# Performance work log

Hardware: AMD Instinct MI355X
Metric: run time of the kernel (lower is better)

The kernel has to match this reference:

```python
import jax, jax.numpy as jnp
import numpy as np

B = 4096
D_IN = 2048
D_H = 2048
W_SCALE = 0.02  # keep exp() gate pre-activations small / numerically safe


def setup_inputs() -> dict:
    key = jax.random.key(0)
    ks = jax.random.split(key, 16)
    inp = {
        "x": jax.random.normal(ks[0], (B, D_IN), jnp.float32),
        "h_prev": jax.random.normal(ks[1], (B, D_H), jnp.float32),
        "c_prev": jax.random.normal(ks[2], (B, D_H), jnp.float32),
        "n_prev": jax.random.uniform(ks[3], (B, D_H), jnp.float32),
    }
    # input->hidden weights (stored [in, out]; torch Linear computes x @ W.T + b,
    # equivalent to x @ W_here + b) and biases
    for i, name in enumerate(["i", "f", "o", "z"]):
        inp[f"W_{name}"] = jax.random.normal(ks[4 + i], (D_IN, D_H), jnp.float32) * W_SCALE
        inp[f"b_{name}"] = jax.random.normal(ks[8 + i], (D_H,), jnp.float32) * W_SCALE
        inp[f"U_{name}"] = jax.random.normal(ks[12 + i], (D_H, D_H), jnp.float32) * W_SCALE
    return inp


def reference(x, h_prev, c_prev, n_prev,
              W_i, b_i, U_i, W_f, b_f, U_f,
              W_o, b_o, U_o, W_z, b_z, U_z):
    # Gate pre-activations: 8 GEMMs fused pairwise per gate
    i = jnp.exp(x @ W_i + b_i + h_prev @ U_i)
    f = jnp.exp(x @ W_f + b_f + h_prev @ U_f)
    o = jax.nn.sigmoid(x @ W_o + b_o + h_prev @ U_o)
    z = jnp.tanh(x @ W_z + b_z + h_prev @ U_z)
    c = f * c_prev + i * z
    n = f * n_prev + i
    h = o * (c / (n + 1e-6))
    return (h, c, n)
```

## Files before the change

### kernel.cpp

```cpp
#include <hip/hip_runtime.h>
#include <hip/hip_bf16.h>
#include <stdint.h>

#define B_DIM 4096
#define DH    2048
#define K_DIM 4096
#define N_DIM 8192
#define NT    128

typedef __bf16  bf16x8 __attribute__((ext_vector_type(8)));
typedef float   f32x4  __attribute__((ext_vector_type(4)));

__device__ __forceinline__ unsigned short f2bf(float f) {
  unsigned int u = __float_as_uint(f);
  u += 0x7FFFu + ((u >> 16) & 1u);
  return (unsigned short)(u >> 16);
}

__global__ void cast_cat_A(const float* __restrict__ x, const float* __restrict__ h,
                           unsigned short* __restrict__ Abuf) {
  int idx = blockIdx.x * 256 + threadIdx.x;
  const int half = B_DIM * (DH / 4);
  bool isx = (idx < half);
  int i2 = isx ? idx : idx - half;
  int b  = i2 >> 9;
  int c4 = i2 & 511;
  const float* src = (isx ? x : h) + (((size_t)b) << 11) + (c4 << 2);
  float4 v = *(const float4*)src;
  ushort4 o;
  o.x = f2bf(v.x); o.y = f2bf(v.y); o.z = f2bf(v.z); o.w = f2bf(v.w);
  int col = (isx ? 0 : DH) + (c4 << 2);
  *(ushort4*)(Abuf + (size_t)b * K_DIM + col) = o;
}

__global__ void transpose_cast_B(const float* __restrict__ Wi, const float* __restrict__ Ui,
                                 const float* __restrict__ Wf, const float* __restrict__ Uf,
                                 const float* __restrict__ Wo, const float* __restrict__ Uo,
                                 const float* __restrict__ Wz, const float* __restrict__ Uz,
                                 unsigned short* __restrict__ Bt) {
  __shared__ unsigned short lds[64 * 68];
  const int k0 = blockIdx.x * 64;
  const int g  = blockIdx.y >> 5;
  const int j0 = (blockIdx.y & 31) * 64;
  const float* W = (g == 0) ? Wi : (g == 1) ? Wf : (g == 2) ? Wo : Wz;
  const float* U = (g == 0) ? Ui : (g == 1) ? Uf : (g == 2) ? Uo : Uz;
  const float* src = ((k0 < DH) ? (W + (size_t)k0 * DH)
                                : (U + (size_t)(k0 - DH) * DH)) + j0;
  const int t = threadIdx.x;
  #pragma unroll
  for (int r = 0; r < 4; ++r) {
    int slot = r * 256 + t;
    int kk = slot >> 4;
    int c4 = slot & 15;
    float4 v = *(const float4*)(src + (size_t)kk * DH + (c4 << 2));
    int n = c4 << 2;
    lds[(n + 0) * 68 + kk] = f2bf(v.x);
    lds[(n + 1) * 68 + kk] = f2bf(v.y);
    lds[(n + 2) * 68 + kk] = f2bf(v.z);
    lds[(n + 3) * 68 + kk] = f2bf(v.w);
  }
  __syncthreads();
  #pragma unroll
  for (int r = 0; r < 4; ++r) {
    int slot = r * 256 + t;
    int nn = slot >> 4;
    int c8 = slot & 15;
    int j  = j0 + nn;
    int np = ((j >> 5) << 7) + ((j & 16) << 2) + (g << 4) + (j & 15);
    *(ushort4*)(Bt + (size_t)np * K_DIM + k0 + (c8 << 2)) =
        *(const ushort4*)(lds + nn * 68 + (c8 << 2));
  }
}

__global__ __launch_bounds__(512, 2) void gemm_gates(const unsigned short* __restrict__ A,
                                                     const unsigned short* __restrict__ Bt,
                                                     const float* __restrict__ bi, const float* __restrict__ bf,
                                                     const float* __restrict__ bo, const float* __restrict__ bz,
                                                     const float* __restrict__ cprev, const float* __restrict__ nprev,
                                                     float* __restrict__ out) {
  __shared__ alignas(16) unsigned short lds[65536];
  unsigned short* As = lds;
  unsigned short* Bs = lds + 32768;

  const int t    = threadIdx.x;
  const int w    = t >> 6;
  const int lane = t & 63;
  const int lm   = lane & 15;
  const int kg   = lane >> 4;
  const int wm   = w >> 2;
  const int wn   = w & 3;

  const int flat = blockIdx.y * 32 + blockIdx.x;
  const int swzb = (flat & 7) * 64 + (flat >> 3);
  const int bx   = swzb & 31;
  const int by   = swzb >> 5;
  const int m0   = by * 256;
  const int n0   = bx * 256;

  const int r4 = lane >> 2, c4 = lane & 3;
  const int rowS0 = w * 32 + r4;
  const int rowS1 = rowS0 + 16;
  const int kby0 = (c4 * 16) ^ (((rowS0 >> 1) & 3) << 4);
  const int kby1 = (c4 * 16) ^ (((rowS1 >> 1) & 3) << 4);
  const unsigned short* pa0 = A  + (size_t)(m0 + rowS0) * K_DIM + (kby0 >> 1);
  const unsigned short* pa1 = A  + (size_t)(m0 + rowS1) * K_DIM + (kby1 >> 1);
  const unsigned short* pb0 = Bt + (size_t)(n0 + rowS0) * K_DIM + (kby0 >> 1);
  const unsigned short* pb1 = Bt + (size_t)(n0 + rowS1) * K_DIM + (kby1 >> 1);
  const int ldsQ0 = (w * 32) * 32;
  const int ldsQ1 = (w * 32 + 16) * 32;

  const int aoff = (wm * 128 + lm) * 64 + ((kg * 16) ^ (((lm >> 1) & 3) << 4));
  const int boff = (wn * 64  + lm) * 64 + ((kg * 16) ^ (((lm >> 1) & 3) << 4));
  const char* Asc = (const char*)As;
  const char* Bsc = (const char*)Bs;

  f32x4 acc[8][4] = {};

#define STAGE(tile) do {                                                                              \
    const int _buf = (tile) & 3;                                                                      \
    const size_t _k = (size_t)(tile) * 32;                                                            \
    __builtin_amdgcn_global_load_lds((const __attribute__((address_space(1))) unsigned int*)(pa0 + _k), \
        (__attribute__((address_space(3))) unsigned int*)(As + _buf * 8192 + ldsQ0), 16, 0, 0);       \
    __builtin_amdgcn_global_load_lds((const __attribute__((address_space(1))) unsigned int*)(pa1 + _k), \
        (__attribute__((address_space(3))) unsigned int*)(As + _buf * 8192 + ldsQ1), 16, 0, 0);       \
    __builtin_amdgcn_global_load_lds((const __attribute__((address_space(1))) unsigned int*)(pb0 + _k), \
        (__attribute__((address_space(3))) unsigned int*)(Bs + _buf * 8192 + ldsQ0), 16, 0, 0);       \
    __builtin_amdgcn_global_load_lds((const __attribute__((address_space(1))) unsigned int*)(pb1 + _k), \
        (__attribute__((address_space(3))) unsigned int*)(Bs + _buf * 8192 + ldsQ1), 16, 0, 0);       \
  } while (0)

  STAGE(0); STAGE(1); STAGE(2);
  asm volatile("s_waitcnt vmcnt(8)" ::: "memory");
  __builtin_amdgcn_s_barrier();
  asm volatile("" ::: "memory");

  for (int kt = 0; kt < NT; ++kt) {
    const int cur = kt & 3;
    if (kt + 3 < NT) STAGE(kt + 3);

    const char* ab = Asc + cur * 16384 + aoff;
    const char* bb = Bsc + cur * 16384 + boff;

    bf16x8 av[4], bv[4];
    #pragma unroll
    for (int ni = 0; ni < 4; ++ni) bv[ni] = *(const bf16x8*)(bb + ni * 1024);

    #pragma unroll
    for (int i = 0; i < 4; ++i) av[i] = *(const bf16x8*)(ab + i * 1024);
    __builtin_amdgcn_s_setprio(1);
    #pragma unroll
    for (int i = 0; i < 4; ++i)
      #pragma unroll
      for (int ni = 0; ni < 4; ++ni)
        acc[i][ni] = __builtin_amdgcn_mfma_f32_16x16x32_bf16(av[i], bv[ni], acc[i][ni], 0, 0, 0);
    __builtin_amdgcn_s_setprio(0);

    #pragma unroll
    for (int i = 0; i < 4; ++i) av[i] = *(const bf16x8*)(ab + 4096 + i * 1024);
    __builtin_amdgcn_s_setprio(1);
    #pragma unroll
    for (int i = 0; i < 4; ++i)
      #pragma unroll
      for (int ni = 0; ni < 4; ++ni)
        acc[4 + i][ni] = __builtin_amdgcn_mfma_f32_16x16x32_bf16(av[i], bv[ni], acc[4 + i][ni], 0, 0, 0);
    __builtin_amdgcn_s_setprio(0);

    if (kt + 3 < NT)      asm volatile("s_waitcnt vmcnt(8)" ::: "memory");
    else if (kt + 2 < NT) asm volatile("s_waitcnt vmcnt(4)" ::: "memory");
    else                  asm volatile("s_waitcnt vmcnt(0)" ::: "memory");
    __builtin_amdgcn_s_barrier();
    asm volatile("" ::: "memory");
  }

  const int jj = bx * 64 + (wn >> 1) * 32 + (wn & 1) * 16 + lm;
  const float vbi = bi[jj], vbf = bf[jj], vbo = bo[jj], vbz = bz[jj];
  #pragma unroll
  for (int mi = 0; mi < 8; ++mi) {
    const int mrow = m0 + wm * 128 + mi * 16 + kg * 4;
    #pragma unroll
    for (int r = 0; r < 4; ++r) {
      const size_t idx = (size_t)(mrow + r) * DH + jj;
      float pi = acc[mi][0][r] + vbi;
      float pf = acc[mi][1][r] + vbf;
      float po = acc[mi][2][r] + vbo;
      float pz = acc[mi][3][r] + vbz;
      float iv = __expf(pi);
      float fv = __expf(pf);
      float ov = 1.0f / (1.0f + __expf(-po));
      float t2 = __expf(2.0f * pz);
      float zv = 1.0f - 2.0f / (t2 + 1.0f);
      float cv = fv * cprev[idx] + iv * zv;
      float nv = fv * nprev[idx] + iv;
      out[idx]            = ov * (cv / (nv + 1e-6f));
      out[8388608 + idx]  = cv;
      out[16777216 + idx] = nv;
    }
  }
#undef STAGE
}

extern "C" void kernel_launch(void* const* d_in, const int* in_sizes, int n_in,
                              void* d_out, int out_size, void* d_ws, size_t ws_size,
                              hipStream_t stream) {
  const float* x      = (const float*)d_in[0];
  const float* h_prev = (const float*)d_in[1];
  const float* c_prev = (const float*)d_in[2];
  const float* n_prev = (const float*)d_in[3];
  const float* W_i = (const float*)d_in[4];  const float* b_i = (const float*)d_in[5];  const float* U_i = (const float*)d_in[6];
  const float* W_f = (const float*)d_in[7];  const float* b_f = (const float*)d_in[8];  const float* U_f = (const float*)d_in[9];
  const float* W_o = (const float*)d_in[10]; const float* b_o = (const float*)d_in[11]; const float* U_o = (const float*)d_in[12];
  const float* W_z = (const float*)d_in[13]; const float* b_z = (const float*)d_in[14]; const float* U_z = (const float*)d_in[15];
  float* out = (float*)d_out;

  char* ws = (char*)d_ws;
  unsigned short* Abuf = (unsigned short*)ws;
  unsigned short* Bt   = (unsigned short*)(ws + 33554432);

  cast_cat_A<<<16384, 256, 0, stream>>>(x, h_prev, Abuf);
  transpose_cast_B<<<dim3(64, 128), 256, 0, stream>>>(W_i, U_i, W_f, U_f, W_o, U_o, W_z, U_z, Bt);
  gemm_gates<<<dim3(32, 16), 512, 0, stream>>>(Abuf, Bt, b_i, b_f, b_o, b_z, c_prev, n_prev, out);
}
```

Measured before the change: 557.5 us.

## Split global-to-LDS staging around MFMA phases and vectorize transpose LDS writes

Measured after the change: 571.6 us. +2.5%, slower.

```diff
diff --git a/kernel.cpp b/kernel.cpp
--- a/kernel.cpp
+++ b/kernel.cpp
@@ -46,18 +46,22 @@
   const float* U = (g == 0) ? Ui : (g == 1) ? Uf : (g == 2) ? Uo : Uz;
   const float* src = ((k0 < DH) ? (W + (size_t)k0 * DH)
                                 : (U + (size_t)(k0 - DH) * DH)) + j0;
-  const int t = threadIdx.x;
-  #pragma unroll
-  for (int r = 0; r < 4; ++r) {
-    int slot = r * 256 + t;
-    int kk = slot >> 4;
-    int c4 = slot & 15;
-    float4 v = *(const float4*)(src + (size_t)kk * DH + (c4 << 2));
-    int n = c4 << 2;
-    lds[(n + 0) * 68 + kk] = f2bf(v.x);
-    lds[(n + 1) * 68 + kk] = f2bf(v.y);
-    lds[(n + 2) * 68 + kk] = f2bf(v.z);
-    lds[(n + 3) * 68 + kk] = f2bf(v.w);
+  const int t  = threadIdx.x;
+  const int tk = t >> 4;
+  const int tj = t & 15;
+  float4 v[4];
+  #pragma unroll
+  for (int r = 0; r < 4; ++r)
+    v[r] = *(const float4*)(src + (size_t)(tk * 4 + r) * DH + tj * 4);
+  #pragma unroll
+  for (int jq = 0; jq < 4; ++jq) {
+    int n = tj * 4 + jq;
+    ushort4 w;
+    w.x = f2bf(((const float*)&v[0])[jq]);
+    w.y = f2bf(((const float*)&v[1])[jq]);
+    w.z = f2bf(((const float*)&v[2])[jq]);
+    w.w = f2bf(((const float*)&v[3])[jq]);
+    *(ushort4*)(lds + n * 68 + tk * 4) = w;
   }
   __syncthreads();
   #pragma unroll
@@ -116,37 +120,41 @@
 
   f32x4 acc[8][4] = {};
 
-#define STAGE(tile) do {                                                                              \
+#define STAGE_A(tile) do {                                                                            \
     const int _buf = (tile) & 3;                                                                      \
     const size_t _k = (size_t)(tile) * 32;                                                            \
     __builtin_amdgcn_global_load_lds((const __attribute__((address_space(1))) unsigned int*)(pa0 + _k), \
         (__attribute__((address_space(3))) unsigned int*)(As + _buf * 8192 + ldsQ0), 16, 0, 0);       \
     __builtin_amdgcn_global_load_lds((const __attribute__((address_space(1))) unsigned int*)(pa1 + _k), \
         (__attribute__((address_space(3))) unsigned int*)(As + _buf * 8192 + ldsQ1), 16, 0, 0);       \
+  } while (0)
+#define STAGE_B(tile) do {                                                                            \
+    const int _buf = (tile) & 3;                                                                      \
+    const size_t _k = (size_t)(tile) * 32;                                                            \
     __builtin_amdgcn_global_load_lds((const __attribute__((address_space(1))) unsigned int*)(pb0 + _k), \
         (__attribute__((address_space(3))) unsigned int*)(Bs + _buf * 8192 + ldsQ0), 16, 0, 0);       \
     __builtin_amdgcn_global_load_lds((const __attribute__((address_space(1))) unsigned int*)(pb1 + _k), \
         (__attribute__((address_space(3))) unsigned int*)(Bs + _buf * 8192 + ldsQ1), 16, 0, 0);       \
   } while (0)
 
-  STAGE(0); STAGE(1); STAGE(2);
+  STAGE_A(0); STAGE_B(0); STAGE_A(1); STAGE_B(1); STAGE_A(2); STAGE_B(2);
   asm volatile("s_waitcnt vmcnt(8)" ::: "memory");
   __builtin_amdgcn_s_barrier();
   asm volatile("" ::: "memory");
 
   for (int kt = 0; kt < NT; ++kt) {
     const int cur = kt & 3;
-    if (kt + 3 < NT) STAGE(kt + 3);
-
     const char* ab = Asc + cur * 16384 + aoff;
     const char* bb = Bsc + cur * 16384 + boff;
-
     bf16x8 av[4], bv[4];
+
     #pragma unroll
     for (int ni = 0; ni < 4; ++ni) bv[ni] = *(const bf16x8*)(bb + ni * 1024);
-
     #pragma unroll
     for (int i = 0; i < 4; ++i) av[i] = *(const bf16x8*)(ab + i * 1024);
+    if (kt + 3 < NT) STAGE_A(kt + 3);
+    __builtin_amdgcn_s_barrier();
+    asm volatile("s_waitcnt lgkmcnt(0)" ::: "memory");
     __builtin_amdgcn_s_setprio(1);
     #pragma unroll
     for (int i = 0; i < 4; ++i)
@@ -154,9 +162,14 @@
       for (int ni = 0; ni < 4; ++ni)
         acc[i][ni] = __builtin_amdgcn_mfma_f32_16x16x32_bf16(av[i], bv[ni], acc[i][ni], 0, 0, 0);
     __builtin_amdgcn_s_setprio(0);
+    __builtin_amdgcn_s_barrier();
+    asm volatile("" ::: "memory");
 
     #pragma unroll
     for (int i = 0; i < 4; ++i) av[i] = *(const bf16x8*)(ab + 4096 + i * 1024);
+    if (kt + 3 < NT) STAGE_B(kt + 3);
+    __builtin_amdgcn_s_barrier();
+    asm volatile("s_waitcnt lgkmcnt(0)" ::: "memory");
     __builtin_amdgcn_s_setprio(1);
     #pragma unroll
     for (int i = 0; i < 4; ++i)
@@ -164,7 +177,6 @@
       for (int ni = 0; ni < 4; ++ni)
         acc[4 + i][ni] = __builtin_amdgcn_mfma_f32_16x16x32_bf16(av[i], bv[ni], acc[4 + i][ni], 0, 0, 0);
     __builtin_amdgcn_s_setprio(0);
-
     if (kt + 3 < NT)      asm volatile("s_waitcnt vmcnt(8)" ::: "memory");
     else if (kt + 2 < NT) asm volatile("s_waitcnt vmcnt(4)" ::: "memory");
     else                  asm volatile("s_waitcnt vmcnt(0)" ::: "memory");
@@ -196,7 +208,8 @@
       out[16777216 + idx] = nv;
     }
   }
-#undef STAGE
+#undef STAGE_A
+#undef STAGE_B
 }
 
 extern "C" void kernel_launch(void* const* d_in, const int* in_sizes, int n_in,
```

## Merge A-cast and B-transpose prep kernels; restage GEMM prefetch after LDS reads

Applied to the files above, without the earlier changes.

Result: no change. 551.0 us (-1.2%).

```diff
diff --git a/kernel.cpp b/kernel.cpp
--- a/kernel.cpp
+++ b/kernel.cpp
@@ -17,58 +17,69 @@
   return (unsigned short)(u >> 16);
 }
 
-__global__ void cast_cat_A(const float* __restrict__ x, const float* __restrict__ h,
-                           unsigned short* __restrict__ Abuf) {
-  int idx = blockIdx.x * 256 + threadIdx.x;
-  const int half = B_DIM * (DH / 4);
-  bool isx = (idx < half);
-  int i2 = isx ? idx : idx - half;
-  int b  = i2 >> 9;
-  int c4 = i2 & 511;
-  const float* src = (isx ? x : h) + (((size_t)b) << 11) + (c4 << 2);
-  float4 v = *(const float4*)src;
-  ushort4 o;
-  o.x = f2bf(v.x); o.y = f2bf(v.y); o.z = f2bf(v.z); o.w = f2bf(v.w);
-  int col = (isx ? 0 : DH) + (c4 << 2);
-  *(ushort4*)(Abuf + (size_t)b * K_DIM + col) = o;
-}
-
-__global__ void transpose_cast_B(const float* __restrict__ Wi, const float* __restrict__ Ui,
-                                 const float* __restrict__ Wf, const float* __restrict__ Uf,
-                                 const float* __restrict__ Wo, const float* __restrict__ Uo,
-                                 const float* __restrict__ Wz, const float* __restrict__ Uz,
-                                 unsigned short* __restrict__ Bt) {
-  __shared__ unsigned short lds[64 * 68];
-  const int k0 = blockIdx.x * 64;
-  const int g  = blockIdx.y >> 5;
-  const int j0 = (blockIdx.y & 31) * 64;
-  const float* W = (g == 0) ? Wi : (g == 1) ? Wf : (g == 2) ? Wo : Wz;
-  const float* U = (g == 0) ? Ui : (g == 1) ? Uf : (g == 2) ? Uo : Uz;
-  const float* src = ((k0 < DH) ? (W + (size_t)k0 * DH)
-                                : (U + (size_t)(k0 - DH) * DH)) + j0;
-  const int t = threadIdx.x;
-  #pragma unroll
-  for (int r = 0; r < 4; ++r) {
-    int slot = r * 256 + t;
-    int kk = slot >> 4;
-    int c4 = slot & 15;
-    float4 v = *(const float4*)(src + (size_t)kk * DH + (c4 << 2));
-    int n = c4 << 2;
-    lds[(n + 0) * 68 + kk] = f2bf(v.x);
-    lds[(n + 1) * 68 + kk] = f2bf(v.y);
-    lds[(n + 2) * 68 + kk] = f2bf(v.z);
-    lds[(n + 3) * 68 + kk] = f2bf(v.w);
-  }
-  __syncthreads();
-  #pragma unroll
-  for (int r = 0; r < 4; ++r) {
-    int slot = r * 256 + t;
-    int nn = slot >> 4;
-    int c8 = slot & 15;
-    int j  = j0 + nn;
-    int np = ((j >> 5) << 7) + ((j & 16) << 2) + (g << 4) + (j & 15);
-    *(ushort4*)(Bt + (size_t)np * K_DIM + k0 + (c8 << 2)) =
-        *(const ushort4*)(lds + nn * 68 + (c8 << 2));
+__global__ __launch_bounds__(256) void prep(const float* __restrict__ x, const float* __restrict__ h,
+                                            unsigned short* __restrict__ Abuf,
+                                            const float* __restrict__ Wi, const float* __restrict__ Ui,
+                                            const float* __restrict__ Wf, const float* __restrict__ Uf,
+                                            const float* __restrict__ Wo, const float* __restrict__ Uo,
+                                            const float* __restrict__ Wz, const float* __restrict__ Uz,
+                                            unsigned short* __restrict__ Bt) {
+  const int bid = blockIdx.x;
+  const int t   = threadIdx.x;
+  if (bid < 8192) {
+    __shared__ unsigned short lds[64 * 68];
+    const int k0 = (bid & 63) * 64;
+    const int gy = bid >> 6;
+    const int g  = gy >> 5;
+    const int j0 = (gy & 31) * 64;
+    const float* W = (g == 0) ? Wi : (g == 1) ? Wf : (g == 2) ? Wo : Wz;
+    const float* U = (g == 0) ? Ui : (g == 1) ? Uf : (g == 2) ? Uo : Uz;
+    const float* src = ((k0 < DH) ? (W + (size_t)k0 * DH)
+                                  : (U + (size_t)(k0 - DH) * DH)) + j0;
+    const int tk = t >> 4;
+    const int tj = t & 15;
+    float4 v[4];
+    #pragma unroll
+    for (int r = 0; r < 4; ++r)
+      v[r] = *(const float4*)(src + (size_t)(tk * 4 + r) * DH + tj * 4);
+    #pragma unroll
+    for (int jq = 0; jq < 4; ++jq) {
+      int n = tj * 4 + jq;
+      ushort4 wv;
+      wv.x = f2bf(((const float*)&v[0])[jq]);
+      wv.y = f2bf(((const float*)&v[1])[jq]);
+      wv.z = f2bf(((const float*)&v[2])[jq]);
+      wv.w = f2bf(((const float*)&v[3])[jq]);
+      *(ushort4*)(lds + n * 68 + tk * 4) = wv;
+    }
+    __syncthreads();
+    #pragma unroll
+    for (int r = 0; r < 4; ++r) {
+      int slot = r * 256 + t;
+      int nn = slot >> 4;
+      int c8 = slot & 15;
+      int j  = j0 + nn;
+      int np = ((j >> 5) << 7) + ((j & 16) << 2) + (g << 4) + (j & 15);
+      *(ushort4*)(Bt + (size_t)np * K_DIM + k0 + (c8 << 2)) =
+          *(const ushort4*)(lds + nn * 68 + (c8 << 2));
+    }
+  } else {
+    const int cb   = bid - 8192;
+    const int half = B_DIM * (DH / 4);
+    #pragma unroll
+    for (int it = 0; it < 16; ++it) {
+      int idx = cb * 4096 + it * 256 + t;
+      bool isx = (idx < half);
+      int i2 = isx ? idx : idx - half;
+      int b  = i2 >> 9;
+      int c4 = i2 & 511;
+      const float* src = (isx ? x : h) + (((size_t)b) << 11) + (c4 << 2);
+      float4 v = *(const float4*)src;
+      ushort4 o;
+      o.x = f2bf(v.x); o.y = f2bf(v.y); o.z = f2bf(v.z); o.w = f2bf(v.w);
+      int col = (isx ? 0 : DH) + (c4 << 2);
+      *(ushort4*)(Abuf + (size_t)b * K_DIM + col) = o;
+    }
   }
 }
 
@@ -136,17 +147,16 @@
 
   for (int kt = 0; kt < NT; ++kt) {
     const int cur = kt & 3;
-    if (kt + 3 < NT) STAGE(kt + 3);
-
     const char* ab = Asc + cur * 16384 + aoff;
     const char* bb = Bsc + cur * 16384 + boff;
-
     bf16x8 av[4], bv[4];
+
     #pragma unroll
     for (int ni = 0; ni < 4; ++ni) bv[ni] = *(const bf16x8*)(bb + ni * 1024);
 
     #pragma unroll
     for (int i = 0; i < 4; ++i) av[i] = *(const bf16x8*)(ab + i * 1024);
+    if (kt + 3 < NT) STAGE(kt + 3);
     __builtin_amdgcn_s_setprio(1);
     #pragma unroll
     for (int i = 0; i < 4; ++i)
@@ -172,14 +182,16 @@
     asm volatile("" ::: "memory");
   }
 
-  const int jj = bx * 64 + (wn >> 1) * 32 + (wn & 1) * 16 + lm;
-  const float vbi = bi[jj], vbf = bf[jj], vbo = bo[jj], vbz = bz[jj];
+  const int jj = (bx << 5) + ((wn >> 1) << 4) + lm;
+  const int jj2 = bx * 64 + (wn >> 1) * 32 + (wn & 1) * 16 + lm;
+  (void)jj;
+  const float vbi = bi[jj2], vbf = bf[jj2], vbo = bo[jj2], vbz = bz[jj2];
   #pragma unroll
   for (int mi = 0; mi < 8; ++mi) {
     const int mrow = m0 + wm * 128 + mi * 16 + kg * 4;
     #pragma unroll
     for (int r = 0; r < 4; ++r) {
-      const size_t idx = (size_t)(mrow + r) * DH + jj;
+      const size_t idx = (size_t)(mrow + r) * DH + jj2;
       float pi = acc[mi][0][r] + vbi;
       float pf = acc[mi][1][r] + vbf;
       float po = acc[mi][2][r] + vbo;
@@ -216,7 +228,7 @@
   unsigned short* Abuf = (unsigned short*)ws;
   unsigned short* Bt   = (unsigned short*)(ws + 33554432);
 
-  cast_cat_A<<<16384, 256, 0, stream>>>(x, h_prev, Abuf);
-  transpose_cast_B<<<dim3(64, 128), 256, 0, stream>>>(W_i, U_i, W_f, U_f, W_o, U_o, W_z, U_z, Bt);
+  prep<<<9216, 256, 0, stream>>>(x, h_prev, Abuf,
+                                 W_i, U_i, W_f, U_f, W_o, U_o, W_z, U_z, Bt);
   gemm_gates<<<dim3(32, 16), 512, 0, stream>>>(Abuf, Bt, b_i, b_f, b_o, b_z, c_prev, n_prev, out);
 }
```
